# Performance work log

Measured on AMD Instinct MI355X. Metric: run time of the kernel, lower is better.

Reference implementation:

```python
import jax, jax.numpy as jnp
import numpy as np

B, P, R_BAR, WIDTH, ADD_WIDTH, KERNEL_WIDTH = 4096, 1024, 64, 1024, 64, 16
NEG_SLOPE = 0.1

def leaky(x):
    return jnp.where(x > 0, x, NEG_SLOPE * x)

def setup_inputs() -> dict:
    key = jax.random.key(0)
    ks = jax.random.split(key, 16)
    s = lambda fan_in: 1.0 / np.sqrt(fan_in)
    return {
        "x": jax.random.normal(ks[0], (B, P), jnp.float32),
        # PCA layer 1: Linear(p -> r_bar), stored [in, out]
        "W_pca": jax.random.normal(ks[1], (P, R_BAR), jnp.float32) * s(P),
        "b_pca": jnp.zeros((R_BAR,), jnp.float32),
        # relu_stack: Linear(r_bar -> width), Linear(width -> width)
        "W1": jax.random.normal(ks[2], (R_BAR, WIDTH), jnp.float32) * s(R_BAR),
        "b1": jnp.zeros((WIDTH,), jnp.float32),
        "W2": jax.random.normal(ks[3], (WIDTH, WIDTH), jnp.float32) * s(WIDTH),
        "b2": jnp.zeros((WIDTH,), jnp.float32),
        # AdditiveLayer 1: r_bar tiny Linears (kernel_width -> add_width), batched [r, in, out]
        "add1_W": jax.random.normal(ks[4], (R_BAR, KERNEL_WIDTH, ADD_WIDTH), jnp.float32) * s(KERNEL_WIDTH),
        "add1_b": jnp.zeros((R_BAR, ADD_WIDTH), jnp.float32),
        "add1_bias": jnp.zeros((1,), jnp.float32),
        # AdditiveLayer 2: r_bar Linears (add_width -> add_width)
        "add2_W": jax.random.normal(ks[5], (R_BAR, ADD_WIDTH, ADD_WIDTH), jnp.float32) * s(ADD_WIDTH),
        "add2_b": jnp.zeros((R_BAR, ADD_WIDTH), jnp.float32),
        "add2_bias": jnp.zeros((1,), jnp.float32),
        # PCA layer 2: Linear(r_bar*add_width -> r_bar)
        "W_pca2": jax.random.normal(ks[6], (R_BAR * ADD_WIDTH, R_BAR), jnp.float32) * s(R_BAR * ADD_WIDTH),
        "b_pca2": jnp.zeros((R_BAR,), jnp.float32),
        # last layer: Linear(r_bar -> 1)
        "W_last": jax.random.normal(ks[7], (R_BAR, 1), jnp.float32) * s(R_BAR),
        "b_last": jnp.zeros((1,), jnp.float32),
    }

def reference(x, W_pca, b_pca, W1, b1, W2, b2,
              add1_W, add1_b, add1_bias,
              add2_W, add2_b, add2_bias,
              W_pca2, b_pca2, W_last, b_last):
    # PcaLayer 1 (cov/trace bookkeeping does not affect the output)
    t = x @ W_pca + b_pca                                   # [B, r_bar]
    # relu_stack (nn_depth = 2)
    h = leaky(t @ W1 + b1)                                   # [B, width]
    h = leaky(h @ W2 + b2)                                   # [B, width]
    # AdditiveLayer 1: modulo-gather kernel_width cols per slot, batched tiny GEMMs
    idx1 = jnp.arange(R_BAR * KERNEL_WIDTH) % h.shape[1]
    g1 = h[:, idx1].reshape(-1, R_BAR, KERNEL_WIDTH)         # [B, r, kw]
    a = jnp.einsum('brk,rko->bro', g1, add1_W) + add1_b      # [B, r, add_w]
    a = leaky(a.reshape(a.shape[0], -1) + add1_bias)         # [B, r*add_w]
    # AdditiveLayer 2: slices are contiguous (mod is identity) -> plain reshape
    g2 = a.reshape(-1, R_BAR, ADD_WIDTH)
    a2 = jnp.einsum('bri,rio->bro', g2, add2_W) + add2_b
    a2 = leaky(a2.reshape(a2.shape[0], -1) + add2_bias)      # [B, r*add_w]
    # PcaLayer 2 + last layer
    t2 = a2 @ W_pca2 + b_pca2                                # [B, r_bar]
    out = (t2 @ W_last + b_last).reshape(-1, 1)              # [B, 1]
    return out
```

## Files before the change

### kernel.cpp

```cpp
#include <hip/hip_runtime.h>

#define NEG_SLOPE 0.1f

__device__ __forceinline__ float leaky(float v) { return v > 0.0f ? v : NEG_SLOPE * v; }

typedef _Float16 h4_t __attribute__((ext_vector_type(4)));
typedef _Float16 h8_t __attribute__((ext_vector_type(8)));
typedef float f32x4 __attribute__((ext_vector_type(4)));

__device__ __forceinline__ unsigned lds_off(const void* p) {
    return (unsigned)(unsigned long long)p;
}

__device__ __forceinline__ void lgkm0() {
    asm volatile("s_waitcnt lgkmcnt(0)" ::: "memory");
    __builtin_amdgcn_sched_barrier(0);
}

__device__ __forceinline__ h4_t tr16(unsigned addr) {
    h4_t d;
    asm volatile("ds_read_b64_tr_b16 %0, %1" : "=v"(d) : "v"(addr) : "memory");
    return d;
}

__global__ __launch_bounds__(256) void prep_and_splitk(const float* __restrict__ W2,
                                                       const float* __restrict__ W1,
                                                       const float* __restrict__ a1W,
                                                       const float* __restrict__ a2W,
                                                       const float* __restrict__ Wp2,
                                                       const float* __restrict__ x,
                                                       const float* __restrict__ Wpca,
                                                       _Float16* __restrict__ W2T,
                                                       _Float16* __restrict__ W1T,
                                                       _Float16* __restrict__ wpack,
                                                       float* __restrict__ P)
{
    __shared__ float tile[32][33];
    __shared__ alignas(16) float As[32][33];
    __shared__ alignas(16) float Bs[32][64];
    const int b   = blockIdx.x;
    const int tid = threadIdx.x;

    if (b < 1024) {
        const int n0 = (b & 31) * 32, k0 = (b >> 5) * 32;
        const int r = tid >> 3, c4 = (tid & 7) * 4;
        float4 v = *reinterpret_cast<const float4*>(&W2[(size_t)(k0 + r) * 1024 + n0 + c4]);
        tile[r][c4 + 0] = v.x; tile[r][c4 + 1] = v.y;
        tile[r][c4 + 2] = v.z; tile[r][c4 + 3] = v.w;
        __syncthreads();
        h4_t o;
        o[0] = (_Float16)tile[c4 + 0][r]; o[1] = (_Float16)tile[c4 + 1][r];
        o[2] = (_Float16)tile[c4 + 2][r]; o[3] = (_Float16)tile[c4 + 3][r];
        *reinterpret_cast<h4_t*>(&W2T[(size_t)(n0 + r) * 1024 + k0 + c4]) = o;
    } else if (b < 1088) {
        const int b2 = b - 1024;
        const int n0 = (b2 & 31) * 32, k0 = (b2 >> 5) * 32;
        const int r = tid >> 3, c4 = (tid & 7) * 4;
        float4 v = *reinterpret_cast<const float4*>(&W1[(size_t)(k0 + r) * 1024 + n0 + c4]);
        tile[r][c4 + 0] = v.x; tile[r][c4 + 1] = v.y;
        tile[r][c4 + 2] = v.z; tile[r][c4 + 3] = v.w;
        __syncthreads();
        h4_t o;
        o[0] = (_Float16)tile[c4 + 0][r]; o[1] = (_Float16)tile[c4 + 1][r];
        o[2] = (_Float16)tile[c4 + 2][r]; o[3] = (_Float16)tile[c4 + 3][r];
        *reinterpret_cast<h4_t*>(&W1T[(size_t)(n0 + r) * 64 + k0 + c4]) = o;
    } else if (b < 3392) {
        const int idx = (b - 1088) * 256 + tid;
        if (idx < 589824) {
            const int r = idx / 9216, qq = idx % 9216;
            float v;
            if (qq < 1024) {
                int nt = qq >> 8, rem = qq & 255, l = rem >> 2, j = rem & 3;
                int n = nt * 16 + (l & 15), k = (l >> 4) * 4 + j;
                v = a1W[(size_t)r * 1024 + k * 64 + n];
            } else if (qq < 5120) {
                int p = qq - 1024, kt = p >> 11, u = p & 2047, nt = u >> 9, s = u & 511,
                    l = s >> 3, j = s & 7;
                int n = nt * 16 + (l & 15), k = kt * 32 + (l >> 4) * 8 + j;
                v = a2W[(size_t)r * 4096 + k * 64 + n];
            } else {
                int p = qq - 5120, kt = p >> 11, u = p & 2047, nt = u >> 9, s = u & 511,
                    l = s >> 3, j = s & 7;
                int n = nt * 16 + (l & 15), k = kt * 32 + (l >> 4) * 8 + j;
                v = Wp2[((size_t)r * 64 + k) * 64 + n];
            }
            wpack[idx] = (_Float16)v;
        }
    } else {
        const int b2    = b - 3392;
        const int row0  = (b2 & 127) * 32;
        const int kbase = (b2 >> 7) * 128;
        const int r0    = (tid >> 4) * 2;
        const int c0    = (tid & 15) * 4;
        const int am    = tid >> 3;
        const int ak    = (tid & 7) * 4;
        float acc[2][4] = {};

#pragma unroll
        for (int kc = 0; kc < 128; kc += 32) {
            const int k0 = kbase + kc;
            float4 va = *reinterpret_cast<const float4*>(&x[(size_t)(row0 + am) * 1024 + k0 + ak]);
            As[ak + 0][am] = va.x; As[ak + 1][am] = va.y;
            As[ak + 2][am] = va.z; As[ak + 3][am] = va.w;
#pragma unroll
            for (int p = 0; p < 2; ++p) {
                int idx = tid + p * 256;
                int kk  = idx >> 4;
                int nq  = (idx & 15) * 4;
                *reinterpret_cast<float4*>(&Bs[kk][nq]) =
                    *reinterpret_cast<const float4*>(&Wpca[(size_t)(k0 + kk) * 64 + nq]);
            }
            __syncthreads();
#pragma unroll
            for (int k = 0; k < 32; ++k) {
                float a0 = As[k][r0], a1 = As[k][r0 + 1];
                float4 bv = *reinterpret_cast<const float4*>(&Bs[k][c0]);
                acc[0][0] = fmaf(a0, bv.x, acc[0][0]); acc[0][1] = fmaf(a0, bv.y, acc[0][1]);
                acc[0][2] = fmaf(a0, bv.z, acc[0][2]); acc[0][3] = fmaf(a0, bv.w, acc[0][3]);
                acc[1][0] = fmaf(a1, bv.x, acc[1][0]); acc[1][1] = fmaf(a1, bv.y, acc[1][1]);
                acc[1][2] = fmaf(a1, bv.z, acc[1][2]); acc[1][3] = fmaf(a1, bv.w, acc[1][3]);
            }
            __syncthreads();
        }
#pragma unroll
        for (int i = 0; i < 2; ++i) {
            float4 o; o.x = acc[i][0]; o.y = acc[i][1]; o.z = acc[i][2]; o.w = acc[i][3];
            *reinterpret_cast<float4*>(
                &P[((size_t)(b2 >> 7) * 4096 + row0 + r0 + i) * 64 + c0]) = o;
        }
    }
}

__global__ __launch_bounds__(256) void combine_t16(const float* __restrict__ P,
                                                   const float* __restrict__ bias,
                                                   const float* __restrict__ bp2,
                                                   const float* __restrict__ Wl,
                                                   const float* __restrict__ bl,
                                                   _Float16* __restrict__ t16,
                                                   float* __restrict__ out)
{
    const int idx = blockIdx.x * 256 + threadIdx.x;
    float s = bias[idx & 63];
#pragma unroll
    for (int c = 0; c < 8; ++c)
        s += P[(size_t)c * 262144 + idx];
    t16[idx] = (_Float16)s;

    if (idx < 4096) {
        float cst = bl[0];
#pragma unroll
        for (int f = 0; f < 64; ++f)
            cst += bp2[f] * Wl[f];
        out[idx] = cst;
    }
}

__global__ __launch_bounds__(256) void gemm_k64_mfma(const _Float16* __restrict__ A,
                                                     const _Float16* __restrict__ BT,
                                                     const float* __restrict__ bias,
                                                     _Float16* __restrict__ C)
{
    __shared__ alignas(16) _Float16 As[128 * 64];
    __shared__ alignas(16) _Float16 Bs[128 * 64];
    const int tid = threadIdx.x;
    const int l   = tid & 63;
    const int w   = tid >> 6;
    const int wm  = w >> 1;
    const int wn  = w & 1;
    const int bm0 = blockIdx.y * 128;
    const int bn0 = blockIdx.x * 128;
    const int fr  = l & 15;
    const int fg  = l >> 4;
    const int srow  = l >> 3;
    const int sslot = l & 7;

#pragma unroll
    for (int i = 0; i < 4; ++i) {
        const int r0   = w * 32 + i * 8;
        const int rowA = r0 + srow;
        const int slot = sslot ^ (rowA & 7);
        __builtin_amdgcn_global_load_lds(
            (const __attribute__((address_space(1))) void*)&A[(size_t)(bm0 + rowA) * 64 + slot * 8],
            (__attribute__((address_space(3))) void*)&As[r0 * 64], 16, 0, 0);
        __builtin_amdgcn_global_load_lds(
            (const __attribute__((address_space(1))) void*)&BT[(size_t)(bn0 + rowA) * 64 + slot * 8],
            (__attribute__((address_space(3))) void*)&Bs[r0 * 64], 16, 0, 0);
    }
    __syncthreads();

    f32x4 acc[4][4] = {};
#pragma unroll
    for (int ks = 0; ks < 2; ++ks) {
        h8_t af[4], bf[4];
#pragma unroll
        for (int mt = 0; mt < 4; ++mt) {
            int row = wm * 64 + mt * 16 + fr;
            int sg  = ks * 4 + fg;
            af[mt] = *reinterpret_cast<const h8_t*>(&As[row * 64 + ((sg ^ (row & 7)) << 3)]);
        }
#pragma unroll
        for (int nt = 0; nt < 4; ++nt) {
            int row = wn * 64 + nt * 16 + fr;
            int sg  = ks * 4 + fg;
            bf[nt] = *reinterpret_cast<const h8_t*>(&Bs[row * 64 + ((sg ^ (row & 7)) << 3)]);
        }
#pragma unroll
        for (int mt = 0; mt < 4; ++mt)
#pragma unroll
            for (int nt = 0; nt < 4; ++nt)
                acc[mt][nt] = __builtin_amdgcn_mfma_f32_16x16x32_f16(af[mt], bf[nt],
                                                                     acc[mt][nt], 0, 0, 0);
    }

#pragma unroll
    for (int nt = 0; nt < 4; ++nt) {
        const int col = bn0 + wn * 64 + nt * 16 + fr;
        const float bv = bias[col];
#pragma unroll
        for (int mt = 0; mt < 4; ++mt)
#pragma unroll
            for (int rg = 0; rg < 4; ++rg) {
                const int row = bm0 + wm * 64 + mt * 16 + fg * 4 + rg;
                float v = acc[mt][nt][rg] + bv;
                C[(size_t)row * 1024 + col] = (_Float16)fmaxf(v, NEG_SLOPE * v);
            }
    }
}

__global__ __launch_bounds__(256) void gemm_mfma_f16_v2(const _Float16* __restrict__ A,
                                                        const _Float16* __restrict__ BT,
                                                        const float* __restrict__ bias,
                                                        _Float16* __restrict__ h2t)
{
    __shared__ alignas(16) _Float16 As[64 * 64];
    __shared__ alignas(16) _Float16 Bs[128 * 64];
    const int tid = threadIdx.x;
    const int l   = tid & 63;
    const int w   = tid >> 6;
    const int wm  = w >> 1;
    const int wn  = w & 1;
    const int bm0 = blockIdx.y * 64;
    const int bn0 = blockIdx.x * 128;
    const int fr  = l & 15;
    const int fg  = l >> 4;
    const int srow  = l >> 3;
    const int sslot = l & 7;

    f32x4 acc[2][4] = {};

    for (int k0 = 0; k0 < 1024; k0 += 64) {
#pragma unroll
        for (int i = 0; i < 2; ++i) {
            const int r0   = w * 16 + i * 8;
            const int rowA = r0 + srow;
            const int slot = sslot ^ (rowA & 7);
            __builtin_amdgcn_global_load_lds(
                (const __attribute__((address_space(1))) void*)&A[(size_t)(bm0 + rowA) * 1024 + k0 + slot * 8],
                (__attribute__((address_space(3))) void*)&As[r0 * 64], 16, 0, 0);
        }
#pragma unroll
        for (int i = 0; i < 4; ++i) {
            const int r0   = w * 32 + i * 8;
            const int rowB = r0 + srow;
            const int slot = sslot ^ (rowB & 7);
            __builtin_amdgcn_global_load_lds(
                (const __attribute__((address_space(1))) void*)&BT[(size_t)(bn0 + rowB) * 1024 + k0 + slot * 8],
                (__attribute__((address_space(3))) void*)&Bs[r0 * 64], 16, 0, 0);
        }
        __syncthreads();

#pragma unroll
        for (int ks = 0; ks < 2; ++ks) {
            h8_t af[2], bf[4];
#pragma unroll
            for (int mt = 0; mt < 2; ++mt) {
                int row = wm * 32 + mt * 16 + fr;
                int sg  = ks * 4 + fg;
                af[mt] = *reinterpret_cast<const h8_t*>(&As[row * 64 + ((sg ^ (row & 7)) << 3)]);
            }
#pragma unroll
            for (int nt = 0; nt < 4; ++nt) {
                int row = wn * 64 + nt * 16 + fr;
                int sg  = ks * 4 + fg;
                bf[nt] = *reinterpret_cast<const h8_t*>(&Bs[row * 64 + ((sg ^ (row & 7)) << 3)]);
            }
#pragma unroll
            for (int mt = 0; mt < 2; ++mt)
#pragma unroll
                for (int nt = 0; nt < 4; ++nt)
                    acc[mt][nt] = __builtin_amdgcn_mfma_f32_16x16x32_f16(af[mt], bf[nt],
                                                                         acc[mt][nt], 0, 0, 0);
        }
        __syncthreads();
    }

    const int rblk0 = (bm0 >> 4) + wm * 2;
    const int cblk0 = (bn0 >> 4) + wn * 4;
#pragma unroll
    for (int nt = 0; nt < 4; ++nt) {
        const int col = bn0 + wn * 64 + nt * 16 + fr;
        const float bv = bias[col];
#pragma unroll
        for (int mt = 0; mt < 2; ++mt) {
            h4_t pk;
#pragma unroll
            for (int r = 0; r < 4; ++r) {
                float v = acc[mt][nt][r] + bv;
                pk[r] = (_Float16)fmaxf(v, NEG_SLOPE * v);
            }
            *reinterpret_cast<h4_t*>(
                &h2t[(((size_t)(cblk0 + nt) * 256 + rblk0 + mt) * 16 + fr) * 16 + fg * 4]) = pk;
        }
    }
}

#define RCH 4

__global__ __launch_bounds__(256) void fused_tail5b(const _Float16* __restrict__ h2t,
                                                    const _Float16* __restrict__ wpack,
                                                    const float* __restrict__ a1b,
                                                    const float* __restrict__ a1bias,
                                                    const float* __restrict__ a2b,
                                                    const float* __restrict__ a2bias,
                                                    const float* __restrict__ Wl,
                                                    float* __restrict__ out)
{
    __shared__ alignas(16) _Float16 stage[2][11264];
    __shared__ alignas(16) _Float16 act[4][2048];

    const int tid = threadIdx.x;
    const int l = tid & 63, w = tid >> 6;
    const int c = l & 15, q = l >> 4;
    const int row0  = blockIdx.x * 128;
    const int rbase = blockIdx.y * RCH;
    const float b1s = a1bias[0], b2s = a2bias[0];

    const unsigned trl   = l * 8;
    const unsigned abase = lds_off(&act[w][0]);

    float b1v[RCH][4], b2v[RCH][4];
#pragma unroll
    for (int rl = 0; rl < RCH; ++rl)
#pragma unroll
        for (int nt = 0; nt < 4; ++nt) {
            b1v[rl][nt] = a1b[(rbase + rl) * 64 + nt * 16 + c] + b1s;
            b2v[rl][nt] = a2b[(rbase + rl) * 64 + nt * 16 + c] + b2s;
        }
    float wlv[4];
#pragma unroll
    for (int nt = 0; nt < 4; ++nt) wlv[nt] = Wl[nt * 16 + c];

    auto STAGE = [&](int rl, int b) {
        const int r = rbase + rl;
        const _Float16* hsrc = h2t + ((size_t)r * 256 + blockIdx.x * 8) * 256;
        const _Float16* wsrc = wpack + (size_t)r * 9216;
#pragma unroll
        for (int i = 0; i < 6; ++i) {
            const int ch = i * 4 + w;
            if (ch < 22) {
                const _Float16* src = (ch < 4) ? (hsrc + ch * 512) : (wsrc + (ch - 4) * 512);
                __builtin_amdgcn_global_load_lds(
                    (const __attribute__((address_space(1))) void*)(src + l * 8),
                    (__attribute__((address_space(3))) void*)&stage[b][ch * 512], 16, 0, 0);
            }
        }
    };

    STAGE(0, 0);
    __syncthreads();

    f32x4 accT[2][4] = {};
    int cur = 0;

#pragma unroll
    for (int rl = 0; rl < RCH; ++rl) {
        if (rl + 1 < RCH) STAGE(rl + 1, cur ^ 1);

        const _Float16* sp = &stage[cur][0];
        const unsigned sbytes = lds_off(sp);

        h4_t ha0 = tr16(sbytes + (unsigned)(w) * 512 + trl);
        h4_t ha1 = tr16(sbytes + (unsigned)(w + 4) * 512 + trl);
        lgkm0();
        f32x4 pa[2][4];
#pragma unroll
        for (int nt = 0; nt < 4; ++nt) {
            h4_t bf = *reinterpret_cast<const h4_t*>(&sp[2048 + nt * 256 + l * 4]);
            pa[0][nt] = __builtin_amdgcn_mfma_f32_16x16x16f16(ha0, bf, (f32x4){0.f,0.f,0.f,0.f}, 0, 0, 0);
            pa[1][nt] = __builtin_amdgcn_mfma_f32_16x16x16f16(ha1, bf, (f32x4){0.f,0.f,0.f,0.f}, 0, 0, 0);
        }
#pragma unroll
        for (int j = 0; j < 2; ++j)
#pragma unroll
            for (int nt = 0; nt < 4; ++nt) {
                h4_t pk;
#pragma unroll
                for (int rg = 0; rg < 4; ++rg) {
                    float v = pa[j][nt][rg] + b1v[rl][nt];
                    pk[rg] = (_Float16)fmaxf(v, NEG_SLOPE * v);
                }
                const int kk = nt * 16 + c;
                const int hh = (kk >> 2) & 1;
                const int kp = (kk & 3) | ((kk >> 3) << 2);
                *reinterpret_cast<h4_t*>(&act[w][j * 1024 + hh * 512 + kp * 16 + q * 4]) = pk;
            }
        lgkm0();

        h8_t afB[2][2];
#pragma unroll
        for (int j = 0; j < 2; ++j)
#pragma unroll
            for (int kt = 0; kt < 2; ++kt) {
                h4_t lo = tr16(abase + (unsigned)(j * 2048 + kt * 512) + trl);
                h4_t hi = tr16(abase + (unsigned)(j * 2048 + 1024 + kt * 512) + trl);
                afB[j][kt] = __builtin_shufflevector(lo, hi, 0, 1, 2, 3, 4, 5, 6, 7);
            }
        lgkm0();
        f32x4 pb[2][4] = {};
#pragma unroll
        for (int kt = 0; kt < 2; ++kt)
#pragma unroll
            for (int nt = 0; nt < 4; ++nt) {
                h8_t bf = *reinterpret_cast<const h8_t*>(&sp[3072 + kt * 2048 + nt * 512 + l * 8]);
                pb[0][nt] = __builtin_amdgcn_mfma_f32_16x16x32_f16(afB[0][kt], bf, pb[0][nt], 0, 0, 0);
                pb[1][nt] = __builtin_amdgcn_mfma_f32_16x16x32_f16(afB[1][kt], bf, pb[1][nt], 0, 0, 0);
            }
#pragma unroll
        for (int j = 0; j < 2; ++j)
#pragma unroll
            for (int nt = 0; nt < 4; ++nt) {
                h4_t pk;
#pragma unroll
                for (int rg = 0; rg < 4; ++rg) {
                    float v = pb[j][nt][rg] + b2v[rl][nt];
                    pk[rg] = (_Float16)fmaxf(v, NEG_SLOPE * v);
                }
                const int kk = nt * 16 + c;
                const int hh = (kk >> 2) & 1;
                const int kp = (kk & 3) | ((kk >> 3) << 2);
                *reinterpret_cast<h4_t*>(&act[w][j * 1024 + hh * 512 + kp * 16 + q * 4]) = pk;
            }
        lgkm0();

        h8_t afC[2][2];
#pragma unroll
        for (int j = 0; j < 2; ++j)
#pragma unroll
            for (int kt = 0; kt < 2; ++kt) {
                h4_t lo = tr16(abase + (unsigned)(j * 2048 + kt * 512) + trl);
                h4_t hi = tr16(abase + (unsigned)(j * 2048 + 1024 + kt * 512) + trl);
                afC[j][kt] = __builtin_shufflevector(lo, hi, 0, 1, 2, 3, 4, 5, 6, 7);
            }
        lgkm0();
#pragma unroll
        for (int kt = 0; kt < 2; ++kt)
#pragma unroll
            for (int nt = 0; nt < 4; ++nt) {
                h8_t bf = *reinterpret_cast<const h8_t*>(&sp[7168 + kt * 2048 + nt * 512 + l * 8]);
                accT[0][nt] = __builtin_amdgcn_mfma_f32_16x16x32_f16(afC[0][kt], bf, accT[0][nt], 0, 0, 0);
                accT[1][nt] = __builtin_amdgcn_mfma_f32_16x16x32_f16(afC[1][kt], bf, accT[1][nt], 0, 0, 0);
            }

        __syncthreads();
        cur ^= 1;
    }

#pragma unroll
    for (int j = 0; j < 2; ++j)
#pragma unroll
        for (int rg = 0; rg < 4; ++rg) {
            float s = accT[j][0][rg] * wlv[0] + accT[j][1][rg] * wlv[1] +
                      accT[j][2][rg] * wlv[2] + accT[j][3][rg] * wlv[3];
            s += __shfl_xor(s, 1);
            s += __shfl_xor(s, 2);
            s += __shfl_xor(s, 4);
            s += __shfl_xor(s, 8);
            if (c == 0) {
                const int row = row0 + (w + 4 * j) * 16 + q * 4 + rg;
                atomicAdd(&out[row], s);
            }
        }
}

extern "C" void kernel_launch(void* const* d_in, const int* in_sizes, int n_in,
                              void* d_out, int out_size, void* d_ws, size_t ws_size,
                              hipStream_t stream)
{
    const float* x      = (const float*)d_in[0];
    const float* Wpca   = (const float*)d_in[1];
    const float* bpca   = (const float*)d_in[2];
    const float* W1     = (const float*)d_in[3];
    const float* b1     = (const float*)d_in[4];
    const float* W2     = (const float*)d_in[5];
    const float* b2     = (const float*)d_in[6];
    const float* a1W    = (const float*)d_in[7];
    const float* a1b    = (const float*)d_in[8];
    const float* a1bias = (const float*)d_in[9];
    const float* a2W    = (const float*)d_in[10];
    const float* a2b    = (const float*)d_in[11];
    const float* a2bias = (const float*)d_in[12];
    const float* Wp2    = (const float*)d_in[13];
    const float* bp2    = (const float*)d_in[14];
    const float* Wl     = (const float*)d_in[15];
    const float* bl     = (const float*)d_in[16];
    float* out = (float*)d_out;

    char* wsb = (char*)d_ws;
    _Float16* t16   = (_Float16*)(wsb);
    _Float16* h1h   = (_Float16*)(wsb + (1ull  << 20));
    _Float16* h2t   = (_Float16*)(wsb + (9ull  << 20));
    _Float16* W2T   = (_Float16*)(wsb + (17ull << 20));
    _Float16* wpack = (_Float16*)(wsb + (19ull << 20));
    _Float16* W1T   = (_Float16*)(wsb + (21ull << 20));
    float*    tpart = (float*)   (wsb + (9ull  << 20));

    prep_and_splitk<<<dim3(4416), 256, 0, stream>>>(W2, W1, a1W, a2W, Wp2, x, Wpca,
                                                    W2T, W1T, wpack, tpart);
    combine_t16<<<dim3(1024), 256, 0, stream>>>(tpart, bpca, bp2, Wl, bl, t16, out);
    gemm_k64_mfma<<<dim3(8, 32), 256, 0, stream>>>(t16, W1T, b1, h1h);
    gemm_mfma_f16_v2<<<dim3(8, 64), 256, 0, stream>>>(h1h, W2T, b2, h2t);
    fused_tail5b<<<dim3(32, 16), 256, 0, stream>>>(h2t, wpack, a1b, a1bias,
                                                   a2b, a2bias, Wl, out);
}
```

Measured before the change: 63.95 us.

## Fold PCA projection into W1 and run x through a single fp16 MFMA GEMM

Precomputes the product Wpca·W1 (and the fused bias bpca·W1+b1) in the prep kernel. It converts x to fp16 so the first two linear layers become one 4096x1024x1024 MFMA GEMM. This removes the fp32 split-K kernel, its partial-sum buffer and the combine launch. In exchange it adds roughly sixteen times more multiply-add work, an extra pass over x for conversion, and a non-pipelined K loop in the new GEMM. It also rounds x to half precision.

```diff
diff --git a/kernel.cpp b/kernel.cpp
--- a/kernel.cpp
+++ b/kernel.cpp
@@ -1,8 +1,6 @@
 #include <hip/hip_runtime.h>
 
 #define NEG_SLOPE 0.1f
-
-__device__ __forceinline__ float leaky(float v) { return v > 0.0f ? v : NEG_SLOPE * v; }
 
 typedef _Float16 h4_t __attribute__((ext_vector_type(4)));
 typedef _Float16 h8_t __attribute__((ext_vector_type(8)));
@@ -23,25 +21,33 @@
     return d;
 }
 
-__global__ __launch_bounds__(256) void prep_and_splitk(const float* __restrict__ W2,
-                                                       const float* __restrict__ W1,
-                                                       const float* __restrict__ a1W,
-                                                       const float* __restrict__ a2W,
-                                                       const float* __restrict__ Wp2,
-                                                       const float* __restrict__ x,
-                                                       const float* __restrict__ Wpca,
-                                                       _Float16* __restrict__ W2T,
-                                                       _Float16* __restrict__ W1T,
-                                                       _Float16* __restrict__ wpack,
-                                                       float* __restrict__ P)
+#define RCH 4
+
+__global__ __launch_bounds__(256) void prep2(const float* __restrict__ W2,
+                                             const float* __restrict__ W1,
+                                             const float* __restrict__ Wpca,
+                                             const float* __restrict__ bpca,
+                                             const float* __restrict__ b1,
+                                             const float* __restrict__ a1W,
+                                             const float* __restrict__ a2W,
+                                             const float* __restrict__ Wp2,
+                                             const float* __restrict__ x,
+                                             const float* __restrict__ bp2,
+                                             const float* __restrict__ Wl,
+                                             const float* __restrict__ bl,
+                                             _Float16* __restrict__ W2T,
+                                             _Float16* __restrict__ wpack,
+                                             _Float16* __restrict__ WfT,
+                                             _Float16* __restrict__ x16,
+                                             float* __restrict__ bfused,
+                                             float* __restrict__ out)
 {
-    __shared__ float tile[32][33];
-    __shared__ alignas(16) float As[32][33];
-    __shared__ alignas(16) float Bs[32][64];
+    __shared__ alignas(16) char smem[17408];
     const int b   = blockIdx.x;
     const int tid = threadIdx.x;
 
     if (b < 1024) {
+        float (*tile)[33] = reinterpret_cast<float(*)[33]>(smem);
         const int n0 = (b & 31) * 32, k0 = (b >> 5) * 32;
         const int r = tid >> 3, c4 = (tid & 7) * 4;
         float4 v = *reinterpret_cast<const float4*>(&W2[(size_t)(k0 + r) * 1024 + n0 + c4]);
@@ -52,20 +58,8 @@
         o[0] = (_Float16)tile[c4 + 0][r]; o[1] = (_Float16)tile[c4 + 1][r];
         o[2] = (_Float16)tile[c4 + 2][r]; o[3] = (_Float16)tile[c4 + 3][r];
         *reinterpret_cast<h4_t*>(&W2T[(size_t)(n0 + r) * 1024 + k0 + c4]) = o;
-    } else if (b < 1088) {
-        const int b2 = b - 1024;
-        const int n0 = (b2 & 31) * 32, k0 = (b2 >> 5) * 32;
-        const int r = tid >> 3, c4 = (tid & 7) * 4;
-        float4 v = *reinterpret_cast<const float4*>(&W1[(size_t)(k0 + r) * 1024 + n0 + c4]);
-        tile[r][c4 + 0] = v.x; tile[r][c4 + 1] = v.y;
-        tile[r][c4 + 2] = v.z; tile[r][c4 + 3] = v.w;
-        __syncthreads();
-        h4_t o;
-        o[0] = (_Float16)tile[c4 + 0][r]; o[1] = (_Float16)tile[c4 + 1][r];
-        o[2] = (_Float16)tile[c4 + 2][r]; o[3] = (_Float16)tile[c4 + 3][r];
-        *reinterpret_cast<h4_t*>(&W1T[(size_t)(n0 + r) * 64 + k0 + c4]) = o;
-    } else if (b < 3392) {
-        const int idx = (b - 1088) * 256 + tid;
+    } else if (b < 3328) {
+        const int idx = (b - 1024) * 256 + tid;
         if (idx < 589824) {
             const int r = idx / 9216, qq = idx % 9216;
             float v;
@@ -86,67 +80,63 @@
             }
             wpack[idx] = (_Float16)v;
         }
+    } else if (b < 4352) {
+        float (*Ws)[65]  = reinterpret_cast<float(*)[65]>(smem);
+        float (*W1s)[33] = reinterpret_cast<float(*)[33]>(smem + 8448);
+        const int b3 = b - 3328;
+        const int n0 = (b3 & 31) * 32, k0 = (b3 >> 5) * 32;
+        {
+            const int r  = tid >> 3;
+            const int j0 = (tid & 7) * 8;
+            float4 v0 = *reinterpret_cast<const float4*>(&Wpca[(size_t)(k0 + r) * 64 + j0]);
+            float4 v1 = *reinterpret_cast<const float4*>(&Wpca[(size_t)(k0 + r) * 64 + j0 + 4]);
+            Ws[r][j0 + 0] = v0.x; Ws[r][j0 + 1] = v0.y; Ws[r][j0 + 2] = v0.z; Ws[r][j0 + 3] = v0.w;
+            Ws[r][j0 + 4] = v1.x; Ws[r][j0 + 5] = v1.y; Ws[r][j0 + 6] = v1.z; Ws[r][j0 + 7] = v1.w;
+            const int j  = tid >> 2;
+            const int nq = (tid & 3) * 8;
+            float4 w0 = *reinterpret_cast<const float4*>(&W1[(size_t)j * 1024 + n0 + nq]);
+            float4 w1 = *reinterpret_cast<const float4*>(&W1[(size_t)j * 1024 + n0 + nq + 4]);
+            W1s[j][nq + 0] = w0.x; W1s[j][nq + 1] = w0.y; W1s[j][nq + 2] = w0.z; W1s[j][nq + 3] = w0.w;
+            W1s[j][nq + 4] = w1.x; W1s[j][nq + 5] = w1.y; W1s[j][nq + 6] = w1.z; W1s[j][nq + 7] = w1.w;
+        }
+        __syncthreads();
+        const int nl = tid >> 3;
+        const int kq = (tid & 7) * 4;
+        float acc[4] = {0.f, 0.f, 0.f, 0.f};
+#pragma unroll
+        for (int j = 0; j < 64; ++j) {
+            float wv = W1s[j][nl];
+#pragma unroll
+            for (int kk = 0; kk < 4; ++kk)
+                acc[kk] = fmaf(Ws[kq + kk][j], wv, acc[kk]);
+        }
+        h4_t pk;
+        pk[0] = (_Float16)acc[0]; pk[1] = (_Float16)acc[1];
+        pk[2] = (_Float16)acc[2]; pk[3] = (_Float16)acc[3];
+        *reinterpret_cast<h4_t*>(&WfT[(size_t)(n0 + nl) * 1024 + k0 + kq]) = pk;
+    } else if (b < 6400) {
+        const size_t base = (size_t)(b - 4352) * 2048 + (size_t)tid * 8;
+        float4 v0 = *reinterpret_cast<const float4*>(&x[base]);
+        float4 v1 = *reinterpret_cast<const float4*>(&x[base + 4]);
+        h8_t o;
+        o[0] = (_Float16)v0.x; o[1] = (_Float16)v0.y; o[2] = (_Float16)v0.z; o[3] = (_Float16)v0.w;
+        o[4] = (_Float16)v1.x; o[5] = (_Float16)v1.y; o[6] = (_Float16)v1.z; o[7] = (_Float16)v1.w;
+        *reinterpret_cast<h8_t*>(&x16[base]) = o;
+    } else if (b == 6400) {
+        const int n = tid * 4;
+        float a0 = b1[n], a1v = b1[n + 1], a2v = b1[n + 2], a3 = b1[n + 3];
+#pragma unroll
+        for (int j = 0; j < 64; ++j) {
+            float bp = bpca[j];
+            a0  = fmaf(bp, W1[(size_t)j * 1024 + n + 0], a0);
+            a1v = fmaf(bp, W1[(size_t)j * 1024 + n + 1], a1v);
+            a2v = fmaf(bp, W1[(size_t)j * 1024 + n + 2], a2v);
+            a3  = fmaf(bp, W1[(size_t)j * 1024 + n + 3], a3);
+        }
+        float4 o; o.x = a0; o.y = a1v; o.z = a2v; o.w = a3;
+        *reinterpret_cast<float4*>(&bfused[n]) = o;
     } else {
-        const int b2    = b - 3392;
-        const int row0  = (b2 & 127) * 32;
-        const int kbase = (b2 >> 7) * 128;
-        const int r0    = (tid >> 4) * 2;
-        const int c0    = (tid & 15) * 4;
-        const int am    = tid >> 3;
-        const int ak    = (tid & 7) * 4;
-        float acc[2][4] = {};
-
-#pragma unroll
-        for (int kc = 0; kc < 128; kc += 32) {
-            const int k0 = kbase + kc;
-            float4 va = *reinterpret_cast<const float4*>(&x[(size_t)(row0 + am) * 1024 + k0 + ak]);
-            As[ak + 0][am] = va.x; As[ak + 1][am] = va.y;
-            As[ak + 2][am] = va.z; As[ak + 3][am] = va.w;
-#pragma unroll
-            for (int p = 0; p < 2; ++p) {
-                int idx = tid + p * 256;
-                int kk  = idx >> 4;
-                int nq  = (idx & 15) * 4;
-                *reinterpret_cast<float4*>(&Bs[kk][nq]) =
-                    *reinterpret_cast<const float4*>(&Wpca[(size_t)(k0 + kk) * 64 + nq]);
-            }
-            __syncthreads();
-#pragma unroll
-            for (int k = 0; k < 32; ++k) {
-                float a0 = As[k][r0], a1 = As[k][r0 + 1];
-                float4 bv = *reinterpret_cast<const float4*>(&Bs[k][c0]);
-                acc[0][0] = fmaf(a0, bv.x, acc[0][0]); acc[0][1] = fmaf(a0, bv.y, acc[0][1]);
-                acc[0][2] = fmaf(a0, bv.z, acc[0][2]); acc[0][3] = fmaf(a0, bv.w, acc[0][3]);
-                acc[1][0] = fmaf(a1, bv.x, acc[1][0]); acc[1][1] = fmaf(a1, bv.y, acc[1][1]);
-                acc[1][2] = fmaf(a1, bv.z, acc[1][2]); acc[1][3] = fmaf(a1, bv.w, acc[1][3]);
-            }
-            __syncthreads();
-        }
-#pragma unroll
-        for (int i = 0; i < 2; ++i) {
-            float4 o; o.x = acc[i][0]; o.y = acc[i][1]; o.z = acc[i][2]; o.w = acc[i][3];
-            *reinterpret_cast<float4*>(
-                &P[((size_t)(b2 >> 7) * 4096 + row0 + r0 + i) * 64 + c0]) = o;
-        }
-    }
-}
-
-__global__ __launch_bounds__(256) void combine_t16(const float* __restrict__ P,
-                                                   const float* __restrict__ bias,
-                                                   const float* __restrict__ bp2,
-                                                   const float* __restrict__ Wl,
-                                                   const float* __restrict__ bl,
-                                                   _Float16* __restrict__ t16,
-                                                   float* __restrict__ out)
-{
-    const int idx = blockIdx.x * 256 + threadIdx.x;
-    float s = bias[idx & 63];
-#pragma unroll
-    for (int c = 0; c < 8; ++c)
-        s += P[(size_t)c * 262144 + idx];
-    t16[idx] = (_Float16)s;
-
-    if (idx < 4096) {
+        const int idx = (b - 6401) * 256 + tid;
         float cst = bl[0];
 #pragma unroll
         for (int f = 0; f < 64; ++f)
@@ -155,61 +145,71 @@
     }
 }
 
-__global__ __launch_bounds__(256) void gemm_k64_mfma(const _Float16* __restrict__ A,
-                                                     const _Float16* __restrict__ BT,
-                                                     const float* __restrict__ bias,
-                                                     _Float16* __restrict__ C)
+__global__ __launch_bounds__(256) void gemm_h1(const _Float16* __restrict__ A,
+                                               const _Float16* __restrict__ BT,
+                                               const float* __restrict__ bias,
+                                               _Float16* __restrict__ C)
 {
-    __shared__ alignas(16) _Float16 As[128 * 64];
+    __shared__ alignas(16) _Float16 As[64 * 64];
     __shared__ alignas(16) _Float16 Bs[128 * 64];
     const int tid = threadIdx.x;
     const int l   = tid & 63;
     const int w   = tid >> 6;
     const int wm  = w >> 1;
     const int wn  = w & 1;
-    const int bm0 = blockIdx.y * 128;
+    const int bm0 = blockIdx.y * 64;
     const int bn0 = blockIdx.x * 128;
     const int fr  = l & 15;
     const int fg  = l >> 4;
     const int srow  = l >> 3;
     const int sslot = l & 7;
 
-#pragma unroll
-    for (int i = 0; i < 4; ++i) {
-        const int r0   = w * 32 + i * 8;
-        const int rowA = r0 + srow;
-        const int slot = sslot ^ (rowA & 7);
-        __builtin_amdgcn_global_load_lds(
-            (const __attribute__((address_space(1))) void*)&A[(size_t)(bm0 + rowA) * 64 + slot * 8],
-            (__attribute__((address_space(3))) void*)&As[r0 * 64], 16, 0, 0);
-        __builtin_amdgcn_global_load_lds(
-            (const __attribute__((address_space(1))) void*)&BT[(size_t)(bn0 + rowA) * 64 + slot * 8],
-            (__attribute__((address_space(3))) void*)&Bs[r0 * 64], 16, 0, 0);
-    }
-    __syncthreads();
-
-    f32x4 acc[4][4] = {};
-#pragma unroll
-    for (int ks = 0; ks < 2; ++ks) {
-        h8_t af[4], bf[4];
-#pragma unroll
-        for (int mt = 0; mt < 4; ++mt) {
-            int row = wm * 64 + mt * 16 + fr;
-            int sg  = ks * 4 + fg;
-            af[mt] = *reinterpret_cast<const h8_t*>(&As[row * 64 + ((sg ^ (row & 7)) << 3)]);
-        }
-#pragma unroll
-        for (int nt = 0; nt < 4; ++nt) {
-            int row = wn * 64 + nt * 16 + fr;
-            int sg  = ks * 4 + fg;
-            bf[nt] = *reinterpret_cast<const h8_t*>(&Bs[row * 64 + ((sg ^ (row & 7)) << 3)]);
-        }
-#pragma unroll
-        for (int mt = 0; mt < 4; ++mt)
-#pragma unroll
-            for (int nt = 0; nt < 4; ++nt)
-                acc[mt][nt] = __builtin_amdgcn_mfma_f32_16x16x32_f16(af[mt], bf[nt],
-                                                                     acc[mt][nt], 0, 0, 0);
+    f32x4 acc[2][4] = {};
+
+    for (int k0 = 0; k0 < 1024; k0 += 64) {
+#pragma unroll
+        for (int i = 0; i < 2; ++i) {
+            const int r0   = w * 16 + i * 8;
+            const int rowA = r0 + srow;
+            const int slot = sslot ^ (rowA & 7);
+            __builtin_amdgcn_global_load_lds(
+                (const __attribute__((address_space(1))) void*)&A[(size_t)(bm0 + rowA) * 1024 + k0 + slot * 8],
+                (__attribute__((address_space(3))) void*)&As[r0 * 64], 16, 0, 0);
+        }
+#pragma unroll
+        for (int i = 0; i < 4; ++i) {
+            const int r0   = w * 32 + i * 8;
+            const int rowB = r0 + srow;
+            const int slot = sslot ^ (rowB & 7);
+            __builtin_amdgcn_global_load_lds(
+                (const __attribute__((address_space(1))) void*)&BT[(size_t)(bn0 + rowB) * 1024 + k0 + slot * 8],
+                (__attribute__((address_space(3))) void*)&Bs[r0 * 64], 16, 0, 0);
+        }
+        __syncthreads();
+
+#pragma unroll
+        for (int ks = 0; ks < 2; ++ks) {
+            h8_t af[2], bf[4];
+#pragma unroll
+            for (int mt = 0; mt < 2; ++mt) {
+                int row = wm * 32 + mt * 16 + fr;
+                int sg  = ks * 4 + fg;
+                af[mt] = *reinterpret_cast<const h8_t*>(&As[row * 64 + ((sg ^ (row & 7)) << 3)]);
+            }
+#pragma unroll
+            for (int nt = 0; nt < 4; ++nt) {
+                int row = wn * 64 + nt * 16 + fr;
+                int sg  = ks * 4 + fg;
+                bf[nt] = *reinterpret_cast<const h8_t*>(&Bs[row * 64 + ((sg ^ (row & 7)) << 3)]);
+            }
+#pragma unroll
+            for (int mt = 0; mt < 2; ++mt)
+#pragma unroll
+                for (int nt = 0; nt < 4; ++nt)
+                    acc[mt][nt] = __builtin_amdgcn_mfma_f32_16x16x32_f16(af[mt], bf[nt],
+                                                                         acc[mt][nt], 0, 0, 0);
+        }
+        __syncthreads();
     }
 
 #pragma unroll
@@ -217,10 +217,10 @@
         const int col = bn0 + wn * 64 + nt * 16 + fr;
         const float bv = bias[col];
 #pragma unroll
-        for (int mt = 0; mt < 4; ++mt)
+        for (int mt = 0; mt < 2; ++mt)
 #pragma unroll
             for (int rg = 0; rg < 4; ++rg) {
-                const int row = bm0 + wm * 64 + mt * 16 + fg * 4 + rg;
+                const int row = bm0 + wm * 32 + mt * 16 + fg * 4 + rg;
                 float v = acc[mt][nt][rg] + bv;
                 C[(size_t)row * 1024 + col] = (_Float16)fmaxf(v, NEG_SLOPE * v);
             }
@@ -313,8 +313,6 @@
         }
     }
 }
-
-#define RCH 4
 
 __global__ __launch_bounds__(256) void fused_tail5b(const _Float16* __restrict__ h2t,
                                                     const _Float16* __restrict__ wpack,
@@ -506,18 +504,18 @@
     float* out = (float*)d_out;
 
     char* wsb = (char*)d_ws;
-    _Float16* t16   = (_Float16*)(wsb);
-    _Float16* h1h   = (_Float16*)(wsb + (1ull  << 20));
-    _Float16* h2t   = (_Float16*)(wsb + (9ull  << 20));
-    _Float16* W2T   = (_Float16*)(wsb + (17ull << 20));
-    _Float16* wpack = (_Float16*)(wsb + (19ull << 20));
-    _Float16* W1T   = (_Float16*)(wsb + (21ull << 20));
-    float*    tpart = (float*)   (wsb + (9ull  << 20));
-
-    prep_and_splitk<<<dim3(4416), 256, 0, stream>>>(W2, W1, a1W, a2W, Wp2, x, Wpca,
-                                                    W2T, W1T, wpack, tpart);
-    combine_t16<<<dim3(1024), 256, 0, stream>>>(tpart, bpca, bp2, Wl, bl, t16, out);
-    gemm_k64_mfma<<<dim3(8, 32), 256, 0, stream>>>(t16, W1T, b1, h1h);
+    _Float16* x16    = (_Float16*)(wsb);
+    _Float16* h1h    = (_Float16*)(wsb + (8ull  << 20));
+    _Float16* h2t    = (_Float16*)(wsb + (16ull << 20));
+    _Float16* W2T    = (_Float16*)(wsb + (24ull << 20));
+    _Float16* wpack  = (_Float16*)(wsb + (26ull << 20));
+    _Float16* WfT    = (_Float16*)(wsb + (28ull << 20));
+    float*    bfused = (float*)   (wsb + (30ull << 20) + (512ull << 10));
+
+    prep2<<<dim3(6417), 256, 0, stream>>>(W2, W1, Wpca, bpca, b1, a1W, a2W, Wp2,
+                                          x, bp2, Wl, bl,
+                                          W2T, wpack, WfT, x16, bfused, out);
+    gemm_h1<<<dim3(8, 64), 256, 0, stream>>>(x16, WfT, bfused, h1h);
     gemm_mfma_f16_v2<<<dim3(8, 64), 256, 0, stream>>>(h1h, W2T, b2, h2t);
     fused_tail5b<<<dim3(32, 16), 256, 0, stream>>>(h2t, wpack, a1b, a1bias,
                                                    a2b, a2bias, Wl, out);
```

Measured after the change: 62.48 us, median of 2. -2.3%, faster.
